# Kernel optimization log

Measured on AMD Instinct MI355X. Metric: run time of the kernel, lower is better.

Reference implementation:

```python
import jax, jax.numpy as jnp
import numpy as np

B, S, D = 4, 2048, 1024
N_HEAD, D_HEAD = 16, 64


def setup_inputs() -> dict:
    key = jax.random.key(0)
    ks = jax.random.split(key, 9)
    sd = 0.02
    x = jax.random.normal(ks[0], (B, S, D), dtype=jnp.float32)
    # causal mask: True = masked (future positions)
    causal = jnp.triu(jnp.ones((S, S), dtype=bool), k=1)
    attn_mask = jnp.broadcast_to(causal, (B, S, S))
    Wq = jax.random.normal(ks[1], (D, N_HEAD * D_HEAD), dtype=jnp.float32) * sd
    bq = jnp.zeros((N_HEAD * D_HEAD,), dtype=jnp.float32)
    Wk = jax.random.normal(ks[2], (D, N_HEAD * D_HEAD), dtype=jnp.float32) * sd
    bk = jnp.zeros((N_HEAD * D_HEAD,), dtype=jnp.float32)
    Wv = jax.random.normal(ks[3], (D, N_HEAD * D_HEAD), dtype=jnp.float32) * sd
    bv = jnp.zeros((N_HEAD * D_HEAD,), dtype=jnp.float32)
    Wo = jax.random.normal(ks[4], (N_HEAD * D_HEAD, D), dtype=jnp.float32) * sd
    bo = jnp.zeros((D,), dtype=jnp.float32)
    return {"x": x, "attn_mask": attn_mask, "Wq": Wq, "bq": bq,
            "Wk": Wk, "bk": bk, "Wv": Wv, "bv": bv, "Wo": Wo, "bo": bo}


def reference(x, attn_mask, Wq, bq, Wk, bk, Wv, bv, Wo, bo):
    b, s, _ = x.shape
    scale = 1.0 / (D_HEAD ** 0.5)
    # QKV projections -> [b, n_head, s, d_head]
    def split_heads(y):
        return y.reshape(b, s, N_HEAD, D_HEAD).transpose(0, 2, 1, 3)
    q = split_heads(x @ Wq + bq)
    k = split_heads(x @ Wk + bk)
    v = split_heads(x @ Wv + bv)
    scores = jnp.einsum('bhqd,bhkd->bhqk', q, k) * scale
    scores = jnp.where(attn_mask[:, None, :, :], jnp.float32(-1e9), scores)
    attn_prob = jax.nn.softmax(scores, axis=-1)
    context = jnp.einsum('bhqk,bhkd->bhqd', attn_prob, v)
    context = context.transpose(0, 2, 1, 3).reshape(b, s, N_HEAD * D_HEAD)
    output = context @ Wo + bo
    return (output, attn_prob)
```

## Files before the change

### kernel.cpp

```cpp
#include <hip/hip_runtime.h>
#include <hip/hip_bf16.h>

typedef unsigned short u16;
typedef __attribute__((ext_vector_type(8))) short bf16x8;
typedef __attribute__((ext_vector_type(4))) float f32x4;

#define S_LEN  2048
#define DMODEL 1024
#define NHEAD  16
#define DH     64
#define BATCH  4
#define QBLK   128
#define KBLK   64
#define SWZ(row, c) (((c) ^ ((row) & 7)))

__device__ inline u16 f2bf(float f) {
  union { float f; unsigned u; } v; v.f = f;
  unsigned u = v.u;
  return (u16)((u + 0x7FFFu + ((u >> 16) & 1u)) >> 16);
}

__device__ inline f32x4 mfma16(bf16x8 a, bf16x8 b, f32x4 c) {
  return __builtin_amdgcn_mfma_f32_16x16x32_bf16(a, b, c, 0, 0, 0);
}

__device__ inline void gload_lds16(const u16* g, u16* l) {
  __builtin_amdgcn_global_load_lds(
      (const __attribute__((address_space(1))) void*)g,
      (__attribute__((address_space(3))) void*)l, 16, 0, 0);
}

__global__ __launch_bounds__(256) void k_convert_x(const float* __restrict__ x,
                                                   u16* __restrict__ xb) {
  int idx = blockIdx.x * 256 + threadIdx.x;
  const float4* p = (const float4*)(x + (size_t)idx * 8);
  float4 a = p[0], b = p[1];
  bf16x8 o;
  o[0] = (short)f2bf(a.x); o[1] = (short)f2bf(a.y);
  o[2] = (short)f2bf(a.z); o[3] = (short)f2bf(a.w);
  o[4] = (short)f2bf(b.x); o[5] = (short)f2bf(b.y);
  o[6] = (short)f2bf(b.z); o[7] = (short)f2bf(b.w);
  *(bf16x8*)(xb + (size_t)idx * 8) = o;
}

__global__ __launch_bounds__(256) void k_wT4(const float* __restrict__ W0,
                                             const float* __restrict__ W1,
                                             const float* __restrict__ W2,
                                             const float* __restrict__ W3,
                                             u16* __restrict__ WtBase) {
  __shared__ float T[32][33];
  int z = blockIdx.z;
  const float* W = (z == 0) ? W0 : (z == 1) ? W1 : (z == 2) ? W2 : W3;
  u16* Wt = WtBase + (size_t)z * DMODEL * DMODEL;
  int tx = threadIdx.x, ty = threadIdx.y;
  int n0 = blockIdx.x * 32, k0 = blockIdx.y * 32;
  for (int i = 0; i < 4; ++i)
    T[ty + i * 8][tx] = W[(size_t)(k0 + ty + i * 8) * DMODEL + n0 + tx];
  __syncthreads();
  for (int i = 0; i < 4; ++i)
    Wt[(size_t)(n0 + ty + i * 8) * DMODEL + k0 + tx] = f2bf(T[tx][ty + i * 8]);
}

__global__ __launch_bounds__(256) void k_gemm_qkv(const u16* __restrict__ A,
                                                  const u16* __restrict__ Wcat,
                                                  const float* __restrict__ bq,
                                                  const float* __restrict__ bk,
                                                  const float* __restrict__ bv,
                                                  u16* __restrict__ Qh,
                                                  u16* __restrict__ Kh,
                                                  u16* __restrict__ Vc) {
  const int K = 1024;
  __shared__ u16 As[128 * 32];
  __shared__ u16 Bs[128 * 32];
  int tid = threadIdx.x, w = tid >> 6, l = tid & 63;
  int bm = blockIdx.x, bn = blockIdx.y;
  int wr = w >> 1, wc = w & 1;
  f32x4 acc[4][4];
  for (int i = 0; i < 4; ++i)
    for (int j = 0; j < 4; ++j) acc[i][j] = (f32x4){0.f, 0.f, 0.f, 0.f};
  const u16* Ablk = A + (size_t)bm * 128 * K;
  const u16* Bblk = Wcat + (size_t)bn * 128 * K;

  for (int ks = 0; ks < K / 32; ++ks) {
    int k0 = ks * 32;
    __syncthreads();
    for (int r = 0; r < 2; ++r) {
      int c = r * 256 + tid;
      int row = c >> 2, c4 = c & 3;
      gload_lds16(Ablk + (size_t)row * K + k0 + c4 * 8, &As[c * 8]);
      gload_lds16(Bblk + (size_t)row * K + k0 + c4 * 8, &Bs[c * 8]);
    }
    __syncthreads();
    bf16x8 af[4], bfr[4];
    for (int mt = 0; mt < 4; ++mt)
      af[mt] = *(const bf16x8*)&As[(wr * 64 + mt * 16 + (l & 15)) * 32 + (l >> 4) * 8];
    for (int nt = 0; nt < 4; ++nt)
      bfr[nt] = *(const bf16x8*)&Bs[(wc * 64 + nt * 16 + (l & 15)) * 32 + (l >> 4) * 8];
    for (int mt = 0; mt < 4; ++mt)
      for (int nt = 0; nt < 4; ++nt)
        acc[mt][nt] = mfma16(af[mt], bfr[nt], acc[mt][nt]);
  }

  int region = (bn * 128) >> 10;
  const float* bias = (region == 0) ? bq : (region == 1) ? bk : bv;
  u16* dst = (region == 0) ? Qh : (region == 1) ? Kh : Vc;

  for (int mt = 0; mt < 4; ++mt)
    for (int nt = 0; nt < 4; ++nt) {
      int colg = bn * 128 + wc * 64 + nt * 16 + (l & 15);
      int col = colg & 1023;
      float bsv = bias[col];
      for (int r = 0; r < 4; ++r) {
        int row = bm * 128 + wr * 64 + mt * 16 + (l >> 4) * 4 + r;
        float v = acc[mt][nt][r] + bsv;
        if (region == 2) {
          dst[(size_t)row * 1024 + col] = f2bf(v);
        } else {
          int b = row >> 11, s = row & 2047, h = col >> 6, d = col & 63;
          dst[(((size_t)(b * NHEAD + h)) * S_LEN + s) * DH + d] = f2bf(v);
        }
      }
    }
}

__global__ __launch_bounds__(256) void k_gemm_out(const u16* __restrict__ A,
                                                  const u16* __restrict__ Bt,
                                                  const float* __restrict__ bias,
                                                  float* __restrict__ Cout) {
  const int K = 1024, N = 1024;
  __shared__ u16 As[128 * 32];
  __shared__ u16 Bs[128 * 32];
  int tid = threadIdx.x, w = tid >> 6, l = tid & 63;
  int bm = blockIdx.x, bn = blockIdx.y;
  int wr = w >> 1, wc = w & 1;
  f32x4 acc[4][4];
  for (int i = 0; i < 4; ++i)
    for (int j = 0; j < 4; ++j) acc[i][j] = (f32x4){0.f, 0.f, 0.f, 0.f};
  const u16* Ablk = A + (size_t)bm * 128 * K;
  const u16* Bblk = Bt + (size_t)bn * 128 * K;

  for (int ks = 0; ks < K / 32; ++ks) {
    int k0 = ks * 32;
    __syncthreads();
    for (int r = 0; r < 2; ++r) {
      int c = r * 256 + tid;
      int row = c >> 2, c4 = c & 3;
      gload_lds16(Ablk + (size_t)row * K + k0 + c4 * 8, &As[c * 8]);
      gload_lds16(Bblk + (size_t)row * K + k0 + c4 * 8, &Bs[c * 8]);
    }
    __syncthreads();
    bf16x8 af[4], bfr[4];
    for (int mt = 0; mt < 4; ++mt)
      af[mt] = *(const bf16x8*)&As[(wr * 64 + mt * 16 + (l & 15)) * 32 + (l >> 4) * 8];
    for (int nt = 0; nt < 4; ++nt)
      bfr[nt] = *(const bf16x8*)&Bs[(wc * 64 + nt * 16 + (l & 15)) * 32 + (l >> 4) * 8];
    for (int mt = 0; mt < 4; ++mt)
      for (int nt = 0; nt < 4; ++nt)
        acc[mt][nt] = mfma16(af[mt], bfr[nt], acc[mt][nt]);
  }

  for (int mt = 0; mt < 4; ++mt)
    for (int nt = 0; nt < 4; ++nt) {
      int col = bn * 128 + wc * 64 + nt * 16 + (l & 15);
      float bsv = bias[col];
      for (int r = 0; r < 4; ++r) {
        int row = bm * 128 + wr * 64 + mt * 16 + (l >> 4) * 4 + r;
        Cout[(size_t)row * N + col] = acc[mt][nt][r] + bsv;
      }
    }
}

__global__ __launch_bounds__(256) void k_vT(const u16* __restrict__ Vc,
                                            u16* __restrict__ Vt) {
  __shared__ u16 T[64][65];
  int bh = blockIdx.x, st = blockIdx.y;
  int b = bh >> 4, h = bh & 15;
  int s0 = st * 64;
  int tid = threadIdx.x;
  int row = tid >> 2, seg = tid & 3;
  const u16* src = Vc + ((size_t)(b * S_LEN + s0 + row)) * DMODEL + h * DH + seg * 16;
  bf16x8 v0 = *(const bf16x8*)src;
  bf16x8 v1 = *(const bf16x8*)(src + 8);
  for (int i = 0; i < 8; ++i) T[row][seg * 16 + i] = (u16)v0[i];
  for (int i = 0; i < 8; ++i) T[row][seg * 16 + 8 + i] = (u16)v1[i];
  __syncthreads();
  int d = row, sc = seg * 16;
  bf16x8 o0, o1;
  for (int i = 0; i < 8; ++i) o0[i] = (short)T[sc + i][d];
  for (int i = 0; i < 8; ++i) o1[i] = (short)T[sc + 8 + i][d];
  u16* dst = Vt + ((size_t)bh * DH + d) * S_LEN + s0 + sc;
  *(bf16x8*)dst = o0;
  *(bf16x8*)(dst + 8) = o1;
}


#define LOADK(KF, J0)                                                          \
  for (int kk_ = 0; kk_ < 2; ++kk_)                                            \
    for (int nt_ = 0; nt_ < 4; ++nt_)                                          \
      KF[kk_][nt_] = *(const bf16x8*)(Kg + (size_t)((J0) + nt_ * 16 + ln) * DH \
                                      + kk_ * 32 + lg * 8);

#define P1TILE(KF, J0)                                                         \
  {                                                                            \
    const int j0_ = (J0);                                                      \
    f32x4 acc[2][4];                                                           \
    for (int mt = 0; mt < 2; ++mt)                                             \
      for (int nt = 0; nt < 4; ++nt) acc[mt][nt] = (f32x4){0.f, 0.f, 0.f, 0.f};\
    for (int kk = 0; kk < 2; ++kk)                                             \
      for (int mt = 0; mt < 2; ++mt)                                           \
        for (int nt = 0; nt < 4; ++nt)                                         \
          acc[mt][nt] = mfma16(qf[mt][kk], KF[kk][nt], acc[mt][nt]);           \
    bool mask_ = (j0_ >= q0);                                                  \
    for (int mt = 0; mt < 2; ++mt)                                             \
      for (int r = 0; r < 4; ++r) {                                            \
        int rl = w * 32 + mt * 16 + lg * 4 + r;                                \
        float x0 = acc[mt][0][r] * scale2;                                     \
        float x1 = acc[mt][1][r] * scale2;                                     \
        float x2 = acc[mt][2][r] * scale2;                                     \
        float x3 = acc[mt][3][r] * scale2;                                     \
        if (mask_) {                                                           \
          if (j0_ + 0 + ln > q0 + rl) x0 = -1e9f;                              \
          if (j0_ + 16 + ln > q0 + rl) x1 = -1e9f;                             \
          if (j0_ + 32 + ln > q0 + rl) x2 = -1e9f;                             \
          if (j0_ + 48 + ln > q0 + rl) x3 = -1e9f;                             \
        }                                                                      \
        float s = __builtin_amdgcn_exp2f(x0) + __builtin_amdgcn_exp2f(x1) +    \
                  __builtin_amdgcn_exp2f(x2) + __builtin_amdgcn_exp2f(x3);     \
        s += __shfl_xor(s, 1);                                                 \
        s += __shfl_xor(s, 2);                                                 \
        s += __shfl_xor(s, 4);                                                 \
        s += __shfl_xor(s, 8);                                                 \
        lrow[mt][r] += s;                                                      \
      }                                                                        \
  }

__global__ __launch_bounds__(256) void k_attn(const u16* __restrict__ Qh,
                                              const u16* __restrict__ Kh,
                                              const u16* __restrict__ Vt,
                                              float* __restrict__ P,
                                              u16* __restrict__ ctx) {
  __shared__ u16 Ps[QBLK * KBLK];

  int bh = blockIdx.x;
  int qb = gridDim.y - 1 - blockIdx.y;
  int q0 = qb * QBLK;
  int tid = threadIdx.x, w = tid >> 6, l = tid & 63;
  const int lg = l >> 4, ln = l & 15;
  const u16* Qg = Qh + (size_t)bh * S_LEN * DH;
  const u16* Kg = Kh + (size_t)bh * S_LEN * DH;
  const u16* Vg = Vt + (size_t)bh * DH * S_LEN;
  float* Pg = P + (size_t)bh * S_LEN * S_LEN;

  bf16x8 qf[2][2];
  for (int mt = 0; mt < 2; ++mt)
    for (int kk = 0; kk < 2; ++kk)
      qf[mt][kk] = *(const bf16x8*)(Qg + (size_t)(q0 + w * 32 + mt * 16 + ln) * DH +
                                    kk * 32 + lg * 8);

  const int nkb = q0 / KBLK + QBLK / KBLK;
  const float scale2 = 0.18033688011112042f;

  float lrow[2][4];
  for (int mt = 0; mt < 2; ++mt)
    for (int r = 0; r < 4; ++r) lrow[mt][r] = 0.f;

  {
    bf16x8 kfA[2][4], kfB[2][4];
    LOADK(kfA, 0);
    for (int kb = 0; kb < nkb; kb += 2) {
      LOADK(kfB, (kb + 1) * KBLK);
      P1TILE(kfA, kb * KBLK);
      if (kb + 2 < nkb) LOADK(kfA, (kb + 2) * KBLK);
      P1TILE(kfB, (kb + 1) * KBLK);
    }
  }
  float ilrow[2][4];
  for (int mt = 0; mt < 2; ++mt)
    for (int r = 0; r < 4; ++r) ilrow[mt][r] = 1.f / lrow[mt][r];

  f32x4 octx[2][4];
  for (int mt = 0; mt < 2; ++mt)
    for (int nt = 0; nt < 4; ++nt) octx[mt][nt] = (f32x4){0.f, 0.f, 0.f, 0.f};

  for (int kb = 0; kb < nkb; ++kb) {
    int j0 = kb * KBLK;
    bf16x8 kf[2][4], vb[2][4];
    LOADK(kf, j0);
    for (int kk = 0; kk < 2; ++kk)
      for (int nt = 0; nt < 4; ++nt)
        vb[kk][nt] = *(const bf16x8*)(Vg + (size_t)(nt * 16 + ln) * S_LEN + j0 +
                                      kk * 32 + lg * 8);
    f32x4 acc[2][4];
    for (int mt = 0; mt < 2; ++mt)
      for (int nt = 0; nt < 4; ++nt) acc[mt][nt] = (f32x4){0.f, 0.f, 0.f, 0.f};
    for (int kk = 0; kk < 2; ++kk)
      for (int mt = 0; mt < 2; ++mt)
        for (int nt = 0; nt < 4; ++nt)
          acc[mt][nt] = mfma16(qf[mt][kk], kf[kk][nt], acc[mt][nt]);

    bool need_mask = (j0 >= q0);
    for (int mt = 0; mt < 2; ++mt)
      for (int r = 0; r < 4; ++r) {
        int rl = w * 32 + mt * 16 + lg * 4 + r;
        float il = ilrow[mt][r];
        float* prow = Pg + (size_t)(q0 + rl) * S_LEN + j0;
        for (int nt = 0; nt < 4; ++nt) {
          int cl = nt * 16 + ln;
          float v = acc[mt][nt][r] * scale2;
          if (need_mask && (j0 + cl > q0 + rl)) v = -1e9f;
          float p = __builtin_amdgcn_exp2f(v) * il;
          __builtin_nontemporal_store(p, prow + cl);
          Ps[rl * 64 + SWZ(rl, cl >> 3) * 8 + (cl & 7)] = f2bf(p);
        }
      }
    for (int kk = 0; kk < 2; ++kk) {
      bf16x8 pa[2];
      for (int mt = 0; mt < 2; ++mt) {
        int row = w * 32 + mt * 16 + ln;
        pa[mt] = *(const bf16x8*)&Ps[row * 64 + SWZ(row, kk * 4 + lg) * 8];
      }
      for (int mt = 0; mt < 2; ++mt)
        for (int nt = 0; nt < 4; ++nt)
          octx[mt][nt] = mfma16(pa[mt], vb[kk][nt], octx[mt][nt]);
    }
  }

  int jz = nkb * KBLK;
  int ncol4 = (S_LEN - jz) >> 2;
  if (ncol4 > 0) {
    f32x4 z = (f32x4){0.f, 0.f, 0.f, 0.f};
    for (int rr = 0; rr < QBLK; ++rr) {
      float* prow = Pg + (size_t)(q0 + rr) * S_LEN + jz;
      for (int j4 = tid; j4 < ncol4; j4 += 256)
        __builtin_nontemporal_store(z, (f32x4*)(prow + j4 * 4));
    }
  }

  int b = bh >> 4, h = bh & 15;
  for (int mt = 0; mt < 2; ++mt)
    for (int nt = 0; nt < 4; ++nt)
      for (int r = 0; r < 4; ++r) {
        int rl = w * 32 + mt * 16 + lg * 4 + r;
        int d = nt * 16 + ln;
        ctx[((size_t)(b * S_LEN + q0 + rl)) * DMODEL + h * DH + d] =
            f2bf(octx[mt][nt][r]);
      }
}

extern "C" void kernel_launch(void* const* d_in, const int* in_sizes, int n_in,
                              void* d_out, int out_size, void* d_ws, size_t ws_size,
                              hipStream_t stream) {
  (void)in_sizes; (void)n_in; (void)out_size; (void)ws_size;
  const float* x  = (const float*)d_in[0];
  const float* Wq = (const float*)d_in[2];
  const float* bq = (const float*)d_in[3];
  const float* Wk = (const float*)d_in[4];
  const float* bk = (const float*)d_in[5];
  const float* Wv = (const float*)d_in[6];
  const float* bv = (const float*)d_in[7];
  const float* Wo = (const float*)d_in[8];
  const float* bo = (const float*)d_in[9];

  char* ws = (char*)d_ws;
  u16* xb   = (u16*)(ws);
  u16* Wcat = (u16*)(ws + 16777216);
  u16* WoT  = Wcat + 3 * (size_t)DMODEL * DMODEL;
  u16* Qh   = (u16*)(ws + 25165824);
  u16* Kh   = (u16*)(ws + 25165824 + 1 * 16777216);
  u16* Vc   = (u16*)(ws + 25165824 + 2 * 16777216);
  u16* Vt   = (u16*)(ws + 25165824 + 3 * 16777216);
  u16* ctx  = Vc;

  float* outp = (float*)d_out;
  float* Pg = outp + (size_t)BATCH * S_LEN * DMODEL;

  k_convert_x<<<4096, 256, 0, stream>>>(x, xb);
  dim3 wtb(32, 8), wtg(32, 32, 4);
  k_wT4<<<wtg, wtb, 0, stream>>>(Wq, Wk, Wv, Wo, Wcat);
  k_gemm_qkv<<<dim3(64, 24), 256, 0, stream>>>(xb, Wcat, bq, bk, bv, Qh, Kh, Vc);
  k_vT<<<dim3(64, 32), 256, 0, stream>>>(Vc, Vt);
  k_attn<<<dim3(64, 16), 256, 0, stream>>>(Qh, Kh, Vt, Pg, ctx);
  k_gemm_out<<<dim3(64, 8), 256, 0, stream>>>(ctx, WoT, bo, outp);
}
```

Baseline: 495.5 us.

## Double-buffer K fragments in attention pass 2 and remap blocks per XCD

The second attention pass now prefetches the next K tile into a ping-pong register buffer while the current tile's scores are computed, so global load latency is hidden behind MFMA and exp work. The grid is flattened to 1D and remapped so that all query blocks of the same (batch, head) land on the same XCD, which improves L2 reuse of K and V. The remap also drops the previous longest-first ordering of query blocks, which may worsen load balance for the causal workload. Register pressure also rises from the extra K buffer.

```diff
diff --git a/kernel.cpp b/kernel.cpp
--- a/kernel.cpp
+++ b/kernel.cpp
@@ -234,6 +234,49 @@
       }                                                                        \
   }
 
+#define P2TILE(KFC, KFN, KB, PRE)                                              \
+  {                                                                            \
+    const int j0_ = (KB) * KBLK;                                               \
+    bf16x8 vb_[2][4];                                                          \
+    for (int kk = 0; kk < 2; ++kk)                                             \
+      for (int nt = 0; nt < 4; ++nt)                                           \
+        vb_[kk][nt] = *(const bf16x8*)(Vg + (size_t)(nt * 16 + ln) * S_LEN +   \
+                                       j0_ + kk * 32 + lg * 8);                \
+    f32x4 acc[2][4];                                                           \
+    for (int mt = 0; mt < 2; ++mt)                                             \
+      for (int nt = 0; nt < 4; ++nt) acc[mt][nt] = (f32x4){0.f, 0.f, 0.f, 0.f};\
+    for (int kk = 0; kk < 2; ++kk)                                             \
+      for (int mt = 0; mt < 2; ++mt)                                           \
+        for (int nt = 0; nt < 4; ++nt)                                         \
+          acc[mt][nt] = mfma16(qf[mt][kk], KFC[kk][nt], acc[mt][nt]);          \
+    if (PRE) { LOADK(KFN, j0_ + KBLK); }                                       \
+    bool mask_ = (j0_ >= q0);                                                  \
+    for (int mt = 0; mt < 2; ++mt)                                             \
+      for (int r = 0; r < 4; ++r) {                                            \
+        int rl = w * 32 + mt * 16 + lg * 4 + r;                                \
+        float il = ilrow[mt][r];                                               \
+        float* prow = Pg + (size_t)(q0 + rl) * S_LEN + j0_;                    \
+        for (int nt = 0; nt < 4; ++nt) {                                       \
+          int cl = nt * 16 + ln;                                               \
+          float v = acc[mt][nt][r] * scale2;                                   \
+          if (mask_ && (j0_ + cl > q0 + rl)) v = -1e9f;                        \
+          float p = __builtin_amdgcn_exp2f(v) * il;                            \
+          __builtin_nontemporal_store(p, prow + cl);                           \
+          Ps[rl * 64 + SWZ(rl, cl >> 3) * 8 + (cl & 7)] = f2bf(p);             \
+        }                                                                      \
+      }                                                                        \
+    for (int kk = 0; kk < 2; ++kk) {                                           \
+      bf16x8 pa[2];                                                            \
+      for (int mt = 0; mt < 2; ++mt) {                                         \
+        int row = w * 32 + mt * 16 + ln;                                       \
+        pa[mt] = *(const bf16x8*)&Ps[row * 64 + SWZ(row, kk * 4 + lg) * 8];    \
+      }                                                                        \
+      for (int mt = 0; mt < 2; ++mt)                                           \
+        for (int nt = 0; nt < 4; ++nt)                                         \
+          octx[mt][nt] = mfma16(pa[mt], vb_[kk][nt], octx[mt][nt]);            \
+    }                                                                          \
+  }
+
 __global__ __launch_bounds__(256) void k_attn(const u16* __restrict__ Qh,
                                               const u16* __restrict__ Kh,
                                               const u16* __restrict__ Vt,
@@ -241,8 +284,10 @@
                                               u16* __restrict__ ctx) {
   __shared__ u16 Ps[QBLK * KBLK];
 
-  int bh = blockIdx.x;
-  int qb = gridDim.y - 1 - blockIdx.y;
+  int flat = blockIdx.x;
+  int xcd = flat & 7, idx = flat >> 3;
+  int bh = xcd * 8 + (idx >> 4);
+  int qb = idx & 15;
   int q0 = qb * QBLK;
   int tid = threadIdx.x, w = tid >> 6, l = tid & 63;
   const int lg = l >> 4, ln = l & 15;
@@ -282,46 +327,12 @@
   for (int mt = 0; mt < 2; ++mt)
     for (int nt = 0; nt < 4; ++nt) octx[mt][nt] = (f32x4){0.f, 0.f, 0.f, 0.f};
 
-  for (int kb = 0; kb < nkb; ++kb) {
-    int j0 = kb * KBLK;
-    bf16x8 kf[2][4], vb[2][4];
-    LOADK(kf, j0);
-    for (int kk = 0; kk < 2; ++kk)
-      for (int nt = 0; nt < 4; ++nt)
-        vb[kk][nt] = *(const bf16x8*)(Vg + (size_t)(nt * 16 + ln) * S_LEN + j0 +
-                                      kk * 32 + lg * 8);
-    f32x4 acc[2][4];
-    for (int mt = 0; mt < 2; ++mt)
-      for (int nt = 0; nt < 4; ++nt) acc[mt][nt] = (f32x4){0.f, 0.f, 0.f, 0.f};
-    for (int kk = 0; kk < 2; ++kk)
-      for (int mt = 0; mt < 2; ++mt)
-        for (int nt = 0; nt < 4; ++nt)
-          acc[mt][nt] = mfma16(qf[mt][kk], kf[kk][nt], acc[mt][nt]);
-
-    bool need_mask = (j0 >= q0);
-    for (int mt = 0; mt < 2; ++mt)
-      for (int r = 0; r < 4; ++r) {
-        int rl = w * 32 + mt * 16 + lg * 4 + r;
-        float il = ilrow[mt][r];
-        float* prow = Pg + (size_t)(q0 + rl) * S_LEN + j0;
-        for (int nt = 0; nt < 4; ++nt) {
-          int cl = nt * 16 + ln;
-          float v = acc[mt][nt][r] * scale2;
-          if (need_mask && (j0 + cl > q0 + rl)) v = -1e9f;
-          float p = __builtin_amdgcn_exp2f(v) * il;
-          __builtin_nontemporal_store(p, prow + cl);
-          Ps[rl * 64 + SWZ(rl, cl >> 3) * 8 + (cl & 7)] = f2bf(p);
-        }
-      }
-    for (int kk = 0; kk < 2; ++kk) {
-      bf16x8 pa[2];
-      for (int mt = 0; mt < 2; ++mt) {
-        int row = w * 32 + mt * 16 + ln;
-        pa[mt] = *(const bf16x8*)&Ps[row * 64 + SWZ(row, kk * 4 + lg) * 8];
-      }
-      for (int mt = 0; mt < 2; ++mt)
-        for (int nt = 0; nt < 4; ++nt)
-          octx[mt][nt] = mfma16(pa[mt], vb[kk][nt], octx[mt][nt]);
+  {
+    bf16x8 kfA[2][4], kfB[2][4];
+    LOADK(kfA, 0);
+    for (int kb = 0; kb < nkb; kb += 2) {
+      P2TILE(kfA, kfB, kb, 1);
+      P2TILE(kfB, kfA, kb + 1, (kb + 2) < nkb);
     }
   }
 
@@ -379,6 +390,6 @@
   k_wT4<<<wtg, wtb, 0, stream>>>(Wq, Wk, Wv, Wo, Wcat);
   k_gemm_qkv<<<dim3(64, 24), 256, 0, stream>>>(xb, Wcat, bq, bk, bv, Qh, Kh, Vc);
   k_vT<<<dim3(64, 32), 256, 0, stream>>>(Vc, Vt);
-  k_attn<<<dim3(64, 16), 256, 0, stream>>>(Qh, Kh, Vt, Pg, ctx);
+  k_attn<<<dim3(1024), 256, 0, stream>>>(Qh, Kh, Vt, Pg, ctx);
   k_gemm_out<<<dim3(64, 8), 256, 0, stream>>>(ctx, WoT, bo, outp);
 }
```

After: 479.9 us. 3.1% less time.
